# Kernel tuning notes

Hardware: AMD Instinct MI355X
Metric: run time of the kernel (lower is better)

Reference implementation:

```python
import jax, jax.numpy as jnp
import numpy as np

N_NODES = 50000
N_EDGES = 800000
D_FEAT = 96
OUT_DIM = 96


def setup_inputs() -> dict:
    key = jax.random.key(0)
    k1, k2, k3, k4 = jax.random.split(key, 4)
    x = jax.random.normal(k1, (N_NODES, D_FEAT), dtype=jnp.float32)
    W = jax.random.normal(k2, (D_FEAT, OUT_DIM), dtype=jnp.float32) / np.sqrt(D_FEAT)
    b = jnp.zeros((OUT_DIM,), dtype=jnp.float32)
    src = jax.random.randint(k3, (N_EDGES,), 0, N_NODES, dtype=jnp.int64)
    dst = jax.random.randint(k4, (N_EDGES,), 0, N_NODES, dtype=jnp.int64)
    return {"x": x, "W": W, "b": b, "src": src, "dst": dst}


def reference(x, W, b, src, dst):
    # GCNConv: symmetric degree normalization, transform-then-aggregate.
    ones = jnp.ones(src.shape[0], dtype=x.dtype)
    deg_out = jax.ops.segment_sum(ones, src, num_segments=N_NODES)  # [N]
    deg_in = jax.ops.segment_sum(ones, dst, num_segments=N_NODES)   # [N]
    inv_sqrt_out = jnp.where(deg_out > 0, jax.lax.rsqrt(deg_out), 0.0)
    inv_sqrt_in = jnp.where(deg_in > 0, jax.lax.rsqrt(deg_in), 0.0)

    h = x @ W  # [N, out_dim] - transform first (cheap GEMM)
    coef = inv_sqrt_out[src] * inv_sqrt_in[dst]         # [E]
    msg = h[src] * coef[:, None]                         # [E, out_dim] gather
    agg = jax.ops.segment_sum(msg, dst, num_segments=N_NODES)  # scatter-reduce
    return agg + b
```

## Files before the change

kernel.cpp:

```cpp
#include <hip/hip_runtime.h>

#define N_NODES 50000
#define N_EDGES 800000
#define DFEAT 96

#define RBITS  14
#define RSIZE  16384
#define HW4 (RSIZE / 4)
#define NRANGE 4
#define NCHUNK 64
#define CHUNK_E (N_EDGES / NCHUNK)
#define HF_BLOCKS (NRANGE * NCHUNK)
#define NB 196

typedef short bf16x8 __attribute__((ext_vector_type(8)));
typedef float f32x4  __attribute__((ext_vector_type(4)));

__device__ __forceinline__ unsigned bpack(float a, float b) {
    unsigned ua = __float_as_uint(a);
    unsigned ub = __float_as_uint(b);
    ua = (ua + 0x7FFFu + ((ua >> 16) & 1u)) >> 16;
    ub = (ub + 0x7FFFu + ((ub >> 16) & 1u)) >> 16;
    return ua | (ub << 16);
}
__device__ __forceinline__ unsigned short b1(float a) {
    unsigned u = __float_as_uint(a);
    u = (u + 0x7FFFu + ((u >> 16) & 1u)) >> 16;
    return (unsigned short)u;
}

__global__ __launch_bounds__(512) void deg_hist_kernel(
    const int* __restrict__ src, const int* __restrict__ dst,
    unsigned* __restrict__ ptab) {
    __shared__ unsigned hh[HW4];
    int tid = threadIdx.x;
    int r = blockIdx.x & (NRANGE - 1);
    int c = blockIdx.x >> 2;
    for (int i = tid; i < HW4; i += 512) hh[i] = 0;
    __syncthreads();
    int lo = r << RBITS;
    const int4* s4 = (const int4*)(src + c * CHUNK_E);
    const int4* d4 = (const int4*)(dst + c * CHUNK_E);
    for (int i = tid; i < CHUNK_E / 4; i += 512) {
        int4 s = s4[i];
        int4 d = d4[i];
        unsigned a;
        a = (unsigned)(s.x - lo); if (a < RSIZE) atomicAdd(&hh[a >> 2], 1u << ((a & 3) << 3));
        a = (unsigned)(s.y - lo); if (a < RSIZE) atomicAdd(&hh[a >> 2], 1u << ((a & 3) << 3));
        a = (unsigned)(s.z - lo); if (a < RSIZE) atomicAdd(&hh[a >> 2], 1u << ((a & 3) << 3));
        a = (unsigned)(s.w - lo); if (a < RSIZE) atomicAdd(&hh[a >> 2], 1u << ((a & 3) << 3));
        a = (unsigned)(d.x - lo); if (a < RSIZE) atomicAdd(&hh[a >> 2], 0x10u << ((a & 3) << 3));
        a = (unsigned)(d.y - lo); if (a < RSIZE) atomicAdd(&hh[a >> 2], 0x10u << ((a & 3) << 3));
        a = (unsigned)(d.z - lo); if (a < RSIZE) atomicAdd(&hh[a >> 2], 0x10u << ((a & 3) << 3));
        a = (unsigned)(d.w - lo); if (a < RSIZE) atomicAdd(&hh[a >> 2], 0x10u << ((a & 3) << 3));
    }
    __syncthreads();
    unsigned* pt = ptab + ((size_t)blockIdx.x << (RBITS - 2));
    for (int i = tid; i < HW4; i += 512) pt[i] = hh[i];
}

__global__ __launch_bounds__(256) void deg_reduce_kernel(
    const unsigned* __restrict__ ptab, unsigned char* __restrict__ pfx,
    int* __restrict__ deg_out, int* __restrict__ deg_in,
    int* __restrict__ bsum) {
    __shared__ int ws[4];
    int tid = threadIdx.x;
    int n = blockIdx.x * 256 + tid;
    int so = 0, si = 0;
    if (n < N_NODES) {
        int r = n >> RBITS, bin = n & (RSIZE - 1);
        int w = bin >> 2, sh = (bin & 3) << 3;
        #pragma unroll 8
        for (int c = 0; c < NCHUNK; ++c) {
            unsigned v = (ptab[(((size_t)(c * NRANGE + r)) << (RBITS - 2)) + w] >> sh) & 0xffu;
            so += (int)(v & 0xfu);
            pfx[(((size_t)(c * NRANGE + r)) << RBITS) + bin] = (unsigned char)si;
            si += (int)(v >> 4);
        }
        deg_out[n] = so;
        deg_in[n]  = si;
    }
    int v = si;
    #pragma unroll
    for (int off = 32; off; off >>= 1) v += __shfl_down(v, off, 64);
    if ((tid & 63) == 0) ws[tid >> 6] = v;
    __syncthreads();
    if (tid == 0) bsum[blockIdx.x] = ws[0] + ws[1] + ws[2] + ws[3];
}

__global__ __launch_bounds__(256) void scan_final_kernel(
    const int* __restrict__ deg, const int* __restrict__ bsum,
    int* __restrict__ offs, int nb) {
    __shared__ int wsum[4];
    __shared__ int sbase;
    int tid = threadIdx.x, lane = tid & 63, wave = tid >> 6;
    int i = blockIdx.x * 256 + tid;
    int v = (i < N_NODES) ? deg[i] : 0;
    int x = v;
    #pragma unroll
    for (int off = 1; off < 64; off <<= 1) {
        int t = __shfl_up(x, off, 64);
        if (lane >= off) x += t;
    }
    if (lane == 63) wsum[wave] = x;
    if (wave == 0) {
        int s = 0;
        for (int j = lane; j < blockIdx.x; j += 64) s += bsum[j];
        #pragma unroll
        for (int off = 32; off; off >>= 1) s += __shfl_down(s, off, 64);
        if (lane == 0) sbase = s;
    }
    if (blockIdx.x == gridDim.x - 1 && wave == 1) {
        int s = 0;
        for (int j = lane; j < nb; j += 64) s += bsum[j];
        #pragma unroll
        for (int off = 32; off; off >>= 1) s += __shfl_down(s, off, 64);
        if (lane == 0) offs[N_NODES] = s;
    }
    __syncthreads();
    int wb = sbase;
    for (int w = 0; w < wave; ++w) wb += wsum[w];
    if (i < N_NODES) offs[i] = wb + x - v;
}

#define GROWS 128
#define NGB ((N_NODES + GROWS - 1) / GROWS)
#define TLD 104

union FGSm {
    unsigned cur[HW4];
    struct {
        unsigned short WT[96 * TLD];
        unsigned short xA[GROWS * TLD];
    } g;
};

__global__ __launch_bounds__(512) void fill_gemm_kernel(
    const int* __restrict__ src, const int* __restrict__ dst,
    const int* __restrict__ offs, const unsigned char* __restrict__ pfx,
    int* __restrict__ csr_src,
    const float* __restrict__ x, const float* __restrict__ W,
    const int* __restrict__ deg_out, unsigned short* __restrict__ h, int nrows) {
    __shared__ FGSm sm;
    int tid = threadIdx.x;

    if (blockIdx.x < HF_BLOCKS) {
        int r = blockIdx.x & (NRANGE - 1);
        int c = blockIdx.x >> 2;
        int lo = r << RBITS;
        const unsigned* pf = (const unsigned*)(pfx + ((size_t)blockIdx.x << RBITS));
        for (int i = tid; i < HW4; i += 512)
            sm.cur[i] = pf[i];
        __syncthreads();
        const int4* s4 = (const int4*)(src + c * CHUNK_E);
        const int4* d4 = (const int4*)(dst + c * CHUNK_E);
        for (int i = tid; i < CHUNK_E / 4; i += 512) {
            int4 s = s4[i];
            int4 d = d4[i];
            unsigned a, old, rank;
            a = (unsigned)(d.x - lo);
            if (a < RSIZE) {
                old = atomicAdd(&sm.cur[a >> 2], 1u << ((a & 3) << 3));
                rank = (old >> ((a & 3) << 3)) & 0xffu;
                csr_src[offs[lo + a] + rank] = s.x;
            }
            a = (unsigned)(d.y - lo);
            if (a < RSIZE) {
                old = atomicAdd(&sm.cur[a >> 2], 1u << ((a & 3) << 3));
                rank = (old >> ((a & 3) << 3)) & 0xffu;
                csr_src[offs[lo + a] + rank] = s.y;
            }
            a = (unsigned)(d.z - lo);
            if (a < RSIZE) {
                old = atomicAdd(&sm.cur[a >> 2], 1u << ((a & 3) << 3));
                rank = (old >> ((a & 3) << 3)) & 0xffu;
                csr_src[offs[lo + a] + rank] = s.z;
            }
            a = (unsigned)(d.w - lo);
            if (a < RSIZE) {
                old = atomicAdd(&sm.cur[a >> 2], 1u << ((a & 3) << 3));
                rank = (old >> ((a & 3) << 3)) & 0xffu;
                csr_src[offs[lo + a] + rank] = s.w;
            }
        }
        return;
    }

    int r0 = (blockIdx.x - HF_BLOCKS) * GROWS;

    for (int i = tid; i < 48 * 96; i += 512) {
        int k2 = i / 96, n = i - k2 * 96;
        float w0 = W[(size_t)(2 * k2) * 96 + n];
        float w1 = W[(size_t)(2 * k2 + 1) * 96 + n];
        *(unsigned*)&sm.g.WT[n * TLD + 2 * k2] = bpack(w0, w1);
    }
    for (int i = tid; i < GROWS * 24; i += 512) {
        int m = i / 24, k4 = i - m * 24;
        int row = r0 + m; if (row >= nrows) row = nrows - 1;
        float4 v = *(const float4*)&x[(size_t)row * 96 + 4 * k4];
        *(unsigned*)&sm.g.xA[m * TLD + 4 * k4]     = bpack(v.x, v.y);
        *(unsigned*)&sm.g.xA[m * TLD + 4 * k4 + 2] = bpack(v.z, v.w);
    }
    __syncthreads();

    int lane = tid & 63, wave = tid >> 6;
    int m16 = lane & 15;
    int g = lane >> 4;
    int rbase = wave * 16;

    bf16x8 afrag[3];
    #pragma unroll
    for (int ks = 0; ks < 3; ++ks)
        afrag[ks] = *(const bf16x8*)&sm.g.xA[(rbase + m16) * TLD + ks * 32 + g * 8];

    f32x4 acc[6];
    #pragma unroll
    for (int nt = 0; nt < 6; ++nt) {
        f32x4 c = {0.f, 0.f, 0.f, 0.f};
        #pragma unroll
        for (int ks = 0; ks < 3; ++ks) {
            bf16x8 bfrag = *(const bf16x8*)&sm.g.WT[(nt * 16 + m16) * TLD + ks * 32 + g * 8];
            c = __builtin_amdgcn_mfma_f32_16x16x32_bf16(afrag[ks], bfrag, c, 0, 0, 0);
        }
        acc[nt] = c;
    }

    float sc[4];
    #pragma unroll
    for (int r = 0; r < 4; ++r) {
        int row = r0 + rbase + g * 4 + r;
        int d = (row < nrows) ? deg_out[row] : 1;
        sc[r] = (d > 0) ? rsqrtf((float)d) : 0.f;
    }
    #pragma unroll
    for (int nt = 0; nt < 6; ++nt) {
        #pragma unroll
        for (int r = 0; r < 4; ++r) {
            int row = r0 + rbase + g * 4 + r;
            if (row < nrows)
                h[(size_t)row * 96 + nt * 16 + m16] = b1(acc[nt][r] * sc[r]);
        }
    }
}

__device__ __forceinline__ void upadd(float* a, uint4 q) {
    a[0] += __uint_as_float(q.x << 16);
    a[1] += __uint_as_float(q.x & 0xffff0000u);
    a[2] += __uint_as_float(q.y << 16);
    a[3] += __uint_as_float(q.y & 0xffff0000u);
    a[4] += __uint_as_float(q.z << 16);
    a[5] += __uint_as_float(q.z & 0xffff0000u);
    a[6] += __uint_as_float(q.w << 16);
    a[7] += __uint_as_float(q.w & 0xffff0000u);
}

#define AGG_NODES 16
#define IDX_CAP 2048
__global__ __launch_bounds__(256) void agg_kernel(
    const unsigned short* __restrict__ h, const int* __restrict__ csr_src,
    const int* __restrict__ offs, const float* __restrict__ b,
    float* __restrict__ out) {
    __shared__ int sh_idx[IDX_CAP];
    __shared__ int sh_off[AGG_NODES + 1];
    int tid = threadIdx.x;
    int n0 = blockIdx.x * AGG_NODES;
    if (tid <= AGG_NODES) sh_off[tid] = offs[n0 + tid];
    __syncthreads();
    int s0 = sh_off[0];
    int len = sh_off[AGG_NODES] - s0;
    bool lds_ok = (len <= IDX_CAP);
    if (lds_ok) {
        for (int i = tid; i < len; i += 256) sh_idx[i] = csr_src[s0 + i];
    }
    __syncthreads();

    int node = tid >> 4;
    int lane16 = tid & 15;
    int j = lane16 & 3;
    int q = lane16 >> 2;
    int start = sh_off[node], end = sh_off[node + 1];
    float acc[24];
    #pragma unroll
    for (int i = 0; i < 24; ++i) acc[i] = 0.f;
    const uint4* hb = (const uint4*)h;

    int e = start + q;
    for (; e + 4 < end; e += 8) {
        int i0 = lds_ok ? sh_idx[e - s0] : csr_src[e];
        int i1 = lds_ok ? sh_idx[e + 4 - s0] : csr_src[e + 4];
        size_t b0 = (size_t)i0 * 12 + j;
        size_t b1 = (size_t)i1 * 12 + j;
        uint4 q0 = hb[b0], q1 = hb[b0 + 4], q2 = hb[b0 + 8];
        uint4 p0 = hb[b1], p1 = hb[b1 + 4], p2 = hb[b1 + 8];
        upadd(acc + 0, q0); upadd(acc + 8, q1); upadd(acc + 16, q2);
        upadd(acc + 0, p0); upadd(acc + 8, p1); upadd(acc + 16, p2);
    }
    if (e < end) {
        int i0 = lds_ok ? sh_idx[e - s0] : csr_src[e];
        size_t b0 = (size_t)i0 * 12 + j;
        uint4 q0 = hb[b0], q1 = hb[b0 + 4], q2 = hb[b0 + 8];
        upadd(acc + 0, q0); upadd(acc + 8, q1); upadd(acc + 16, q2);
    }
    #pragma unroll
    for (int i = 0; i < 24; ++i) {
        acc[i] += __shfl_xor(acc[i], 4, 64);
        acc[i] += __shfl_xor(acc[i], 8, 64);
    }
    if (q != 0) return;
    float inv = (end > start) ? rsqrtf((float)(end - start)) : 0.f;
    int n = n0 + node;
    #pragma unroll
    for (int g = 0; g < 3; ++g) {
        int slot = j + 4 * g;
        float4 bb0 = *(const float4*)(b + 8 * slot);
        float4 bb1 = *(const float4*)(b + 8 * slot + 4);
        float4 r0, r1;
        r0.x = acc[g * 8 + 0] * inv + bb0.x;
        r0.y = acc[g * 8 + 1] * inv + bb0.y;
        r0.z = acc[g * 8 + 2] * inv + bb0.z;
        r0.w = acc[g * 8 + 3] * inv + bb0.w;
        r1.x = acc[g * 8 + 4] * inv + bb1.x;
        r1.y = acc[g * 8 + 5] * inv + bb1.y;
        r1.z = acc[g * 8 + 6] * inv + bb1.z;
        r1.w = acc[g * 8 + 7] * inv + bb1.w;
        float4* o = (float4*)(out + (size_t)n * DFEAT + 8 * slot);
        o[0] = r0; o[1] = r1;
    }
}

extern "C" void kernel_launch(void* const* d_in, const int* in_sizes, int n_in,
                              void* d_out, int out_size, void* d_ws, size_t ws_size,
                              hipStream_t stream) {
    const float* x  = (const float*)d_in[0];
    const float* W  = (const float*)d_in[1];
    const float* b  = (const float*)d_in[2];
    const int*   src = (const int*)d_in[3];
    const int*   dst = (const int*)d_in[4];
    float* out = (float*)d_out;

    int* deg_out = (int*)d_ws;
    int* deg_in  = deg_out + N_NODES;
    int* offs    = deg_in + N_NODES;
    int* csr_src = offs + N_NODES + 1;
    int* bsum    = csr_src + N_EDGES;
    size_t off1 = (((size_t)(3 * N_NODES + 1 + N_EDGES + 256)) * 4 + 255) & ~(size_t)255;
    unsigned* ptab = (unsigned*)((char*)d_ws + off1);
    size_t off2 = off1 + ((size_t)HF_BLOCKS << (RBITS - 2)) * 4;
    unsigned char* pfx = (unsigned char*)((char*)d_ws + off2);
    size_t off3 = (off2 + ((size_t)HF_BLOCKS << RBITS) + 255) & ~(size_t)255;
    unsigned short* h = (unsigned short*)((char*)d_ws + off3);

    deg_hist_kernel<<<HF_BLOCKS, 512, 0, stream>>>(src, dst, ptab);
    deg_reduce_kernel<<<NB, 256, 0, stream>>>(ptab, pfx, deg_out, deg_in, bsum);
    scan_final_kernel<<<NB, 256, 0, stream>>>(deg_in, bsum, offs, NB);
    fill_gemm_kernel<<<HF_BLOCKS + NGB, 512, 0, stream>>>(
        src, dst, offs, pfx, csr_src, x, W, deg_out, h, N_NODES);
    agg_kernel<<<N_NODES / AGG_NODES, 256, 0, stream>>>(h, csr_src, offs, b, out);
}
```

Baseline: 133.3 us.

## Compact per-range edge pairs in histogram pass to avoid rescanning edges in fill

```diff
diff --git a/kernel.cpp b/kernel.cpp
--- a/kernel.cpp
+++ b/kernel.cpp
@@ -12,6 +12,7 @@
 #define CHUNK_E (N_EDGES / NCHUNK)
 #define HF_BLOCKS (NRANGE * NCHUNK)
 #define NB 196
+#define CAP 4608
 
 typedef short bf16x8 __attribute__((ext_vector_type(8)));
 typedef float f32x4  __attribute__((ext_vector_type(4)));
@@ -31,30 +32,50 @@
 
 __global__ __launch_bounds__(512) void deg_hist_kernel(
     const int* __restrict__ src, const int* __restrict__ dst,
-    unsigned* __restrict__ ptab) {
+    unsigned* __restrict__ ptab, unsigned* __restrict__ pairP,
+    int* __restrict__ pcnt) {
     __shared__ unsigned hh[HW4];
-    int tid = threadIdx.x;
+    __shared__ int cnt;
+    int tid = threadIdx.x, lane = tid & 63;
     int r = blockIdx.x & (NRANGE - 1);
     int c = blockIdx.x >> 2;
     for (int i = tid; i < HW4; i += 512) hh[i] = 0;
+    if (tid == 0) cnt = 0;
     __syncthreads();
     int lo = r << RBITS;
     const int4* s4 = (const int4*)(src + c * CHUNK_E);
     const int4* d4 = (const int4*)(dst + c * CHUNK_E);
-    for (int i = tid; i < CHUNK_E / 4; i += 512) {
-        int4 s = s4[i];
-        int4 d = d4[i];
+    unsigned* pp = pairP + (size_t)blockIdx.x * CAP;
+    const int NIT = (CHUNK_E / 4 + 511) / 512;
+    for (int it = 0; it < NIT; ++it) {
+        int i = it * 512 + tid;
+        bool valid = i < CHUNK_E / 4;
+        int4 s = valid ? s4[i] : make_int4(-1, -1, -1, -1);
+        int4 d = valid ? d4[i] : make_int4(-1, -1, -1, -1);
         unsigned a;
         a = (unsigned)(s.x - lo); if (a < RSIZE) atomicAdd(&hh[a >> 2], 1u << ((a & 3) << 3));
         a = (unsigned)(s.y - lo); if (a < RSIZE) atomicAdd(&hh[a >> 2], 1u << ((a & 3) << 3));
         a = (unsigned)(s.z - lo); if (a < RSIZE) atomicAdd(&hh[a >> 2], 1u << ((a & 3) << 3));
         a = (unsigned)(s.w - lo); if (a < RSIZE) atomicAdd(&hh[a >> 2], 1u << ((a & 3) << 3));
-        a = (unsigned)(d.x - lo); if (a < RSIZE) atomicAdd(&hh[a >> 2], 0x10u << ((a & 3) << 3));
-        a = (unsigned)(d.y - lo); if (a < RSIZE) atomicAdd(&hh[a >> 2], 0x10u << ((a & 3) << 3));
-        a = (unsigned)(d.z - lo); if (a < RSIZE) atomicAdd(&hh[a >> 2], 0x10u << ((a & 3) << 3));
-        a = (unsigned)(d.w - lo); if (a < RSIZE) atomicAdd(&hh[a >> 2], 0x10u << ((a & 3) << 3));
-    }
-    __syncthreads();
+        int dv[4] = {d.x, d.y, d.z, d.w};
+        int sv[4] = {s.x, s.y, s.z, s.w};
+        #pragma unroll
+        for (int k = 0; k < 4; ++k) {
+            unsigned aa = (unsigned)(dv[k] - lo);
+            bool p = aa < RSIZE;
+            if (p) atomicAdd(&hh[aa >> 2], 0x10u << ((aa & 3) << 3));
+            unsigned long long m = __ballot(p);
+            int base = 0;
+            if (lane == 0) base = atomicAdd(&cnt, (int)__popcll(m));
+            base = __shfl(base, 0, 64);
+            if (p) {
+                int slot = base + (int)__popcll(m & ((1ULL << lane) - 1ULL));
+                pp[slot] = (aa << 17) | (unsigned)sv[k];
+            }
+        }
+    }
+    __syncthreads();
+    if (tid == 0) pcnt[blockIdx.x] = cnt;
     unsigned* pt = ptab + ((size_t)blockIdx.x << (RBITS - 2));
     for (int i = tid; i < HW4; i += 512) pt[i] = hh[i];
 }
@@ -136,7 +157,7 @@
 };
 
 __global__ __launch_bounds__(512) void fill_gemm_kernel(
-    const int* __restrict__ src, const int* __restrict__ dst,
+    const unsigned* __restrict__ pairP, const int* __restrict__ pcnt,
     const int* __restrict__ offs, const unsigned char* __restrict__ pfx,
     int* __restrict__ csr_src,
     const float* __restrict__ x, const float* __restrict__ W,
@@ -145,43 +166,20 @@
     int tid = threadIdx.x;
 
     if (blockIdx.x < HF_BLOCKS) {
-        int r = blockIdx.x & (NRANGE - 1);
-        int c = blockIdx.x >> 2;
-        int lo = r << RBITS;
+        int lo = (blockIdx.x & (NRANGE - 1)) << RBITS;
         const unsigned* pf = (const unsigned*)(pfx + ((size_t)blockIdx.x << RBITS));
         for (int i = tid; i < HW4; i += 512)
             sm.cur[i] = pf[i];
         __syncthreads();
-        const int4* s4 = (const int4*)(src + c * CHUNK_E);
-        const int4* d4 = (const int4*)(dst + c * CHUNK_E);
-        for (int i = tid; i < CHUNK_E / 4; i += 512) {
-            int4 s = s4[i];
-            int4 d = d4[i];
-            unsigned a, old, rank;
-            a = (unsigned)(d.x - lo);
-            if (a < RSIZE) {
-                old = atomicAdd(&sm.cur[a >> 2], 1u << ((a & 3) << 3));
-                rank = (old >> ((a & 3) << 3)) & 0xffu;
-                csr_src[offs[lo + a] + rank] = s.x;
-            }
-            a = (unsigned)(d.y - lo);
-            if (a < RSIZE) {
-                old = atomicAdd(&sm.cur[a >> 2], 1u << ((a & 3) << 3));
-                rank = (old >> ((a & 3) << 3)) & 0xffu;
-                csr_src[offs[lo + a] + rank] = s.y;
-            }
-            a = (unsigned)(d.z - lo);
-            if (a < RSIZE) {
-                old = atomicAdd(&sm.cur[a >> 2], 1u << ((a & 3) << 3));
-                rank = (old >> ((a & 3) << 3)) & 0xffu;
-                csr_src[offs[lo + a] + rank] = s.z;
-            }
-            a = (unsigned)(d.w - lo);
-            if (a < RSIZE) {
-                old = atomicAdd(&sm.cur[a >> 2], 1u << ((a & 3) << 3));
-                rank = (old >> ((a & 3) << 3)) & 0xffu;
-                csr_src[offs[lo + a] + rank] = s.w;
-            }
+        int n = pcnt[blockIdx.x];
+        const unsigned* pp = pairP + (size_t)blockIdx.x * CAP;
+        for (int i = tid; i < n; i += 512) {
+            unsigned p = pp[i];
+            unsigned a = p >> 17;
+            int s = (int)(p & 0x1FFFFu);
+            unsigned old = atomicAdd(&sm.cur[a >> 2], 1u << ((a & 3) << 3));
+            unsigned rank = (old >> ((a & 3) << 3)) & 0xffu;
+            csr_src[offs[lo + a] + rank] = s;
         }
         return;
     }
@@ -349,11 +347,15 @@
     unsigned char* pfx = (unsigned char*)((char*)d_ws + off2);
     size_t off3 = (off2 + ((size_t)HF_BLOCKS << RBITS) + 255) & ~(size_t)255;
     unsigned short* h = (unsigned short*)((char*)d_ws + off3);
-
-    deg_hist_kernel<<<HF_BLOCKS, 512, 0, stream>>>(src, dst, ptab);
+    size_t off4 = (off3 + (size_t)N_NODES * DFEAT * 2 + 255) & ~(size_t)255;
+    unsigned* pairP = (unsigned*)((char*)d_ws + off4);
+    size_t off5 = off4 + (size_t)HF_BLOCKS * CAP * 4;
+    int* pcnt = (int*)((char*)d_ws + off5);
+
+    deg_hist_kernel<<<HF_BLOCKS, 512, 0, stream>>>(src, dst, ptab, pairP, pcnt);
     deg_reduce_kernel<<<NB, 256, 0, stream>>>(ptab, pfx, deg_out, deg_in, bsum);
     scan_final_kernel<<<NB, 256, 0, stream>>>(deg_in, bsum, offs, NB);
     fill_gemm_kernel<<<HF_BLOCKS + NGB, 512, 0, stream>>>(
-        src, dst, offs, pfx, csr_src, x, W, deg_out, h, N_NODES);
+        pairP, pcnt, offs, pfx, csr_src, x, W, deg_out, h, N_NODES);
     agg_kernel<<<N_NODES / AGG_NODES, 256, 0, stream>>>(h, csr_src, offs, b, out);
 }
```

Result: slower. 139.1 us (+4.4%).
